# Optimization experiments

Measured on AMD Instinct MI355X. Metric: run time of the kernel, lower is better.

The kernel has to match this reference:

```python
import jax, jax.numpy as jnp
from jax import lax
import numpy as np

EPS = 1e-06


def conv1x1(x, W, b):
    # x: [B,C,H,W], W: [O,C], b: [O]
    return jnp.einsum('bchw,oc->bohw', x, W) + b[None, :, None, None]


def conv3x3(x, W, b):
    # W: [O,I,3,3], 'SAME' padding
    y = lax.conv_general_dilated(x, W, (1, 1), 'SAME',
                                 dimension_numbers=('NCHW', 'OIHW', 'NCHW'))
    return y + b[None, :, None, None]


def setup_inputs() -> dict:
    key = jax.random.key(0)
    ks = jax.random.split(key, 13)
    B, C, H, W = 8, 64, 256, 256
    kc, vc = 64, 64
    s = 0.05
    return {
        'x':  jax.random.normal(ks[0], (B, C, H, W), jnp.float32),
        'Wq': jax.random.normal(ks[1], (kc, C), jnp.float32) * s,
        'bq': jax.random.normal(ks[2], (kc,), jnp.float32) * s,
        'Wk': jax.random.normal(ks[3], (kc, C), jnp.float32) * s,
        'bk': jax.random.normal(ks[4], (kc,), jnp.float32) * s,
        'Wv': jax.random.normal(ks[5], (vc, C), jnp.float32) * s,
        'bv': jax.random.normal(ks[6], (vc,), jnp.float32) * s,
        'Wr': jax.random.normal(ks[7], (C, vc), jnp.float32) * s,
        'br': jax.random.normal(ks[8], (C,), jnp.float32) * s,
        'W1': jax.random.normal(ks[9], (C, C, 3, 3), jnp.float32) * s,
        'b1': jax.random.normal(ks[10], (C,), jnp.float32) * s,
        'W2': jax.random.normal(ks[11], (C, C, 3, 3), jnp.float32) * s,
        'b2': jax.random.normal(ks[12], (C,), jnp.float32) * s,
    }


def reference(x, Wq, bq, Wk, bk, Wv, bv, Wr, br, W1, b1, W2, b2):
    B, C, H, W = x.shape
    N = H * W
    kc = Wq.shape[0]
    vc = Wv.shape[0]

    Q = conv1x1(x, Wq, bq).reshape(B, kc, N)
    K = conv1x1(x, Wk, bk).reshape(B, kc, N)
    V = conv1x1(x, Wv, bv).reshape(B, vc, N)

    # L2-normalize over the channel axis (dim=-2 in torch)
    Qn = Q / jnp.linalg.norm(Q, axis=1, keepdims=True)   # [B,kc,N]
    Kn = K / jnp.linalg.norm(K, axis=1, keepdims=True)   # [B,kc,N]
    Qt = jnp.transpose(Qn, (0, 2, 1))                     # [B,N,kc]

    # denominator: 1 / (N + Q . (sum_n K + eps))
    k_sum = Kn.sum(axis=-1) + EPS                         # [B,kc]
    denom = 1.0 / (N + jnp.einsum('bnc,bc->bn', Qt, k_sum))  # [B,N]

    value_sum = V.sum(axis=-1, keepdims=True)             # [B,vc,1]

    # linear-attention aggregation: KV^T then Q.(KV)
    agg_kv = jnp.einsum('bmn,bcn->bmc', Kn, V)            # [B,kc,vc]
    # the per-batch/per-head torch loop sums head slices of the full kc
    # contraction -> equivalent to a single einsum over kc
    agg_qkv = jnp.einsum('bmc,bnm->bcn', agg_kv, Qt)      # [B,vc,N]

    numerator = value_sum + agg_qkv                       # [B,vc,N]
    weight_value = (numerator * denom[:, None, :]).reshape(B, vc, H, W)

    attn = conv1x1(weight_value, Wr, br)                  # [B,C,H,W]
    out = conv3x3(conv3x3(attn, W1, b1), W2, b2) * x + x
    return out
```

## Files before the change

kernel.cpp:

```cpp
#include <hip/hip_runtime.h>

typedef __attribute__((ext_vector_type(8))) short short8;
typedef __attribute__((ext_vector_type(4))) float f32x4;
typedef __attribute__((ext_vector_type(4))) int i32x4;

#define NPIX 65536
#define KPITCH 264
#define RED_KSUM 0
#define RED_VSUM 512
#define RED_AGG 1024

__device__ __forceinline__ float b2f(unsigned short u) {
  union { unsigned int i; float f; } z; z.i = ((unsigned int)u) << 16; return z.f;
}
__device__ __forceinline__ unsigned short f2b(float f) {
  union { float f; unsigned int i; } z; z.f = f;
  unsigned int r = z.i + 0x7fffu + ((z.i >> 16) & 1u);
  return (unsigned short)(r >> 16);
}
__device__ __forceinline__ unsigned int packbf(float a, float b) {
  return (unsigned int)f2b(a) | ((unsigned int)f2b(b) << 16);
}
__device__ __forceinline__ int cvtpk(float a, float b) {
  int r;
  asm("v_cvt_pk_bf16_f32 %0, %1, %2" : "=v"(r) : "v"(a), "v"(b));
  return r;
}

__global__ __launch_bounds__(256) void prep_kernel(
    const float* __restrict__ W1, const float* __restrict__ W2,
    const float* __restrict__ Wq, const float* __restrict__ Wk,
    const float* __restrict__ Wv,
    unsigned short* __restrict__ wA, unsigned short* __restrict__ wQKV,
    float* __restrict__ red)
{
  const int i = blockIdx.x * 256 + threadIdx.x;
  if (i < 73728) {
    const float* W = (i < 36864) ? W1 : W2;
    const int e = (i < 36864) ? i : (i - 36864);
    const int j    = e & 7;
    const int lane = (e >> 3) & 63;
    const int mt   = (e >> 9) & 3;
    const int kb   = (e >> 11) & 1;
    const int tap  = e >> 12;
    const int o = mt * 16 + (lane & 15);
    const int c = kb * 32 + ((lane >> 4) << 3) + j;
    wA[i] = f2b(W[o * 576 + c * 9 + tap]);
  } else if (i < 86016) {
    const int e = i - 73728;
    const int j    = e & 7;
    const int lane = (e >> 3) & 63;
    const int mt   = (e >> 9) & 3;
    const int kb   = (e >> 11) & 1;
    const int pj   = e >> 12;
    const float* W = (pj == 0) ? Wq : (pj == 1) ? Wk : Wv;
    const int o = mt * 16 + (lane & 15);
    const int c = kb * 32 + ((lane >> 4) << 3) + j;
    wQKV[e] = f2b(W[o * 64 + c]);
  } else if (i < 119808) {
    red[i - 86016] = 0.0f;
  }
}

#define PROJ(PIDX, BM)                                                         \
    {                                                                          \
      _Pragma("unroll")                                                        \
      for (int mt = 0; mt < 4; ++mt) {                                         \
        const f32x4 bb = *(const f32x4*)((BM) + mt * 16 + g * 4);              \
        _Pragma("unroll")                                                      \
        for (int nt = 0; nt < 4; ++nt) acc[mt][nt] = bb;                       \
      }                                                                        \
      _Pragma("unroll")                                                        \
      for (int kb = 0; kb < 2; ++kb) {                                         \
        const unsigned short* wp = wQKV + ((PIDX) * 2 + kb) * 2048 + l * 8;    \
        short8 af[4];                                                          \
        _Pragma("unroll")                                                      \
        for (int mt = 0; mt < 4; ++mt)                                         \
          af[mt] = *(const short8*)(wp + mt * 512);                            \
        _Pragma("unroll")                                                      \
        for (int mt = 0; mt < 4; ++mt)                                         \
          _Pragma("unroll")                                                    \
          for (int nt = 0; nt < 4; ++nt)                                       \
            acc[mt][nt] = __builtin_amdgcn_mfma_f32_16x16x32_bf16(             \
                af[mt], bf[nt][kb], acc[mt][nt], 0, 0, 0);                     \
      }                                                                        \
    }

__global__ __launch_bounds__(256, 2) void qkv_kernel(
    const float* __restrict__ x,
    const unsigned short* __restrict__ wQKV,
    const float* __restrict__ bq, const float* __restrict__ bk,
    const float* __restrict__ bv,
    unsigned short* __restrict__ Qn, float* __restrict__ red)
{
  __shared__ __align__(16) unsigned short sh[2 * 64 * KPITCH];
  unsigned short* ks = sh;
  unsigned short* vs = sh + 64 * KPITCH;
  unsigned int* shu = (unsigned int*)sh;
  const int b = blockIdx.y;
  const int t = threadIdx.x;
  const int w = t >> 6;
  const int l = t & 63;
  const int g = l >> 4;
  const int l15 = l & 15;
  const size_t xb = (size_t)b * 64 * NPIX;

  const f32x4 zero = {0.f, 0.f, 0.f, 0.f};
  f32x4 agg[4]  = {zero, zero, zero, zero};
  f32x4 kacc[4] = {zero, zero, zero, zero};
  f32x4 vacc[4] = {zero, zero, zero, zero};

  for (int it = 0; it < 4; ++it) {
    const int pxw = (blockIdx.x << 10) + (it << 8) + (w << 6);

    short8 bf[4][2];
#pragma unroll
    for (int nt = 0; nt < 4; ++nt) {
      const float* xp = x + xb + (size_t)(g * 8) * NPIX + pxw + nt * 16 + l15;
#pragma unroll
      for (int kb = 0; kb < 2; ++kb) {
        float f[8];
#pragma unroll
        for (int j = 0; j < 8; ++j)
          f[j] = xp[(size_t)(kb * 32 + j) * NPIX];
        union { i32x4 i; short8 s; } u;
        u.i.x = cvtpk(f[0], f[1]); u.i.y = cvtpk(f[2], f[3]);
        u.i.z = cvtpk(f[4], f[5]); u.i.w = cvtpk(f[6], f[7]);
        bf[nt][kb] = u.s;
      }
    }

    f32x4 acc[4][4];

    PROJ(0, bq);
    {
      float rq[4];
#pragma unroll
      for (int nt = 0; nt < 4; ++nt) {
        float ss = 0.f;
#pragma unroll
        for (int mt = 0; mt < 4; ++mt)
#pragma unroll
          for (int r = 0; r < 4; ++r)
            ss = fmaf(acc[mt][nt][r], acc[mt][nt][r], ss);
        ss += __shfl_xor(ss, 16);
        ss += __shfl_xor(ss, 32);
        rq[nt] = rsqrtf(ss);
      }
      unsigned int* sw = shu + w * 2304;
#pragma unroll
      for (int mt = 0; mt < 4; ++mt)
#pragma unroll
        for (int nt = 0; nt < 4; ++nt) {
          const int px = nt * 16 + l15;
          unsigned int* dst = sw + px * 36 + mt * 8 + g * 2;
          dst[0] = (unsigned)cvtpk(acc[mt][nt][0] * rq[nt], acc[mt][nt][1] * rq[nt]);
          dst[1] = (unsigned)cvtpk(acc[mt][nt][2] * rq[nt], acc[mt][nt][3] * rq[nt]);
        }
      const uint4* rr4 = (const uint4*)(shu + w * 2304);
#pragma unroll
      for (int k8 = 0; k8 < 8; ++k8) {
        const int p = (k8 << 3) + (l >> 3);
        const int ch8 = l & 7;
        *(uint4*)(Qn + ((size_t)b * NPIX + pxw + p) * 64 + ch8 * 8) =
            rr4[p * 9 + ch8];
      }
      __syncthreads();
    }

    PROJ(1, bk);
    {
      float rk[4];
#pragma unroll
      for (int nt = 0; nt < 4; ++nt) {
        float ss = 0.f;
#pragma unroll
        for (int mt = 0; mt < 4; ++mt)
#pragma unroll
          for (int r = 0; r < 4; ++r)
            ss = fmaf(acc[mt][nt][r], acc[mt][nt][r], ss);
        ss += __shfl_xor(ss, 16);
        ss += __shfl_xor(ss, 32);
        rk[nt] = rsqrtf(ss);
      }
#pragma unroll
      for (int mt = 0; mt < 4; ++mt)
#pragma unroll
        for (int nt = 0; nt < 4; ++nt)
#pragma unroll
          for (int r = 0; r < 4; ++r) {
            const float kn = acc[mt][nt][r] * rk[nt];
            kacc[mt][r] += kn;
            ks[(mt * 16 + g * 4 + r) * KPITCH + (w << 6) + nt * 16 + l15] =
                (unsigned short)cvtpk(kn, 0.f);
          }
    }

    PROJ(2, bv);
    {
#pragma unroll
      for (int mt = 0; mt < 4; ++mt)
#pragma unroll
        for (int nt = 0; nt < 4; ++nt)
#pragma unroll
          for (int r = 0; r < 4; ++r) {
            const float vv = acc[mt][nt][r];
            vacc[mt][r] += vv;
            vs[(mt * 16 + g * 4 + r) * KPITCH + (w << 6) + nt * 16 + l15] =
                (unsigned short)cvtpk(vv, 0.f);
          }
    }
    __syncthreads();

#pragma unroll
    for (int s = 0; s < 8; ++s) {
      const short8 ak =
          *(const short8*)(ks + (w * 16 + l15) * KPITCH + s * 32 + g * 8);
#pragma unroll
      for (int nt = 0; nt < 4; ++nt) {
        const short8 bv8 =
            *(const short8*)(vs + (nt * 16 + l15) * KPITCH + s * 32 + g * 8);
        agg[nt] = __builtin_amdgcn_mfma_f32_16x16x32_bf16(ak, bv8, agg[nt], 0, 0, 0);
      }
    }
    __syncthreads();
  }

#pragma unroll
  for (int mt = 0; mt < 4; ++mt)
#pragma unroll
    for (int r = 0; r < 4; ++r) {
      float kv = kacc[mt][r], vv = vacc[mt][r];
#pragma unroll
      for (int d = 1; d < 16; d <<= 1) {
        kv += __shfl_xor(kv, d);
        vv += __shfl_xor(vv, d);
      }
      if (l15 == 0) {
        atomicAdd(red + RED_KSUM + b * 64 + mt * 16 + g * 4 + r, kv);
        atomicAdd(red + RED_VSUM + b * 64 + mt * 16 + g * 4 + r, vv);
      }
    }
  float* ab = red + RED_AGG + b * 4096;
#pragma unroll
  for (int nt = 0; nt < 4; ++nt)
#pragma unroll
    for (int r = 0; r < 4; ++r)
      atomicAdd(ab + (w * 16 + g * 4 + r) * 64 + nt * 16 + l15, agg[nt][r]);
}

__global__ __launch_bounds__(256) void prep2_kernel(
    const float* __restrict__ Wr, const float* __restrict__ red,
    unsigned short* __restrict__ Cb, float* __restrict__ u,
    float* __restrict__ ks2)
{
  const int b = blockIdx.y;
  const int t = threadIdx.x;
  const int o = t & 63;
  const int kq = t >> 6;
  const float* wr = Wr + o * 64;
  const float* agg = red + RED_AGG + b * 4096;
#pragma unroll
  for (int i = 0; i < 4; ++i) {
    const int k = blockIdx.x * 16 + kq * 4 + i;
    const float* ar = agg + k * 64;
    float s = 0.f;
#pragma unroll
    for (int v = 0; v < 64; ++v) s = fmaf(wr[v], ar[v], s);
    const int mt = o >> 4, kb = k >> 5;
    const int lane = (o & 15) | (((k >> 3) & 3) << 4);
    const int j = k & 7;
    const unsigned short c1 = f2b(s);
    const float r1 = s - b2f(c1);
    Cb[b * 4096 + ((kb * 4 + mt) * 64 + lane) * 8 + j] = c1;
    Cb[32768 + b * 4096 + ((kb * 4 + mt) * 64 + lane) * 8 + j] = f2b(r1);
  }
  if (blockIdx.x == 0 && t < 64) {
    const float* vsr = red + RED_VSUM + b * 64;
    float s = 0.f;
#pragma unroll
    for (int v = 0; v < 64; ++v) s = fmaf(Wr[t * 64 + v], vsr[v], s);
    u[b * 64 + t] = s;
    ks2[b * 64 + t] = red[RED_KSUM + b * 64 + t] + 1e-6f;
  }
}

__global__ __launch_bounds__(256, 2) void attn_kernel(
    const unsigned short* __restrict__ Qn,
    const unsigned short* __restrict__ Cb,
    const float* __restrict__ u,
    const float* __restrict__ ks2,
    const float* __restrict__ br,
    unsigned short* __restrict__ attn)
{
  __shared__ __align__(16) unsigned short att[256 * 72];
  const int b = blockIdx.y;
  const int t = threadIdx.x;
  const int w = t >> 6, l = t & 63, g = l >> 4, l15 = l & 15;

  short8 af[2][2][4];
#pragma unroll
  for (int lvl = 0; lvl < 2; ++lvl)
#pragma unroll
    for (int kb = 0; kb < 2; ++kb)
#pragma unroll
      for (int mt = 0; mt < 4; ++mt)
        af[lvl][kb][mt] = *(const short8*)(
            Cb + lvl * 32768 + b * 4096 + ((kb * 4 + mt) * 64 + l) * 8);
  f32x4 uu[4], brf[4];
#pragma unroll
  for (int mt = 0; mt < 4; ++mt) {
    uu[mt]  = *(const f32x4*)(u + b * 64 + mt * 16 + g * 4);
    brf[mt] = *(const f32x4*)(br + mt * 16 + g * 4);
  }
  float ksl[16];
#pragma unroll
  for (int kb = 0; kb < 2; ++kb)
#pragma unroll
    for (int j = 0; j < 8; ++j)
      ksl[kb * 8 + j] = ks2[b * 64 + kb * 32 + g * 8 + j];

  for (int it = 0; it < 4; ++it) {
    const int pxw = (blockIdx.x << 10) + (it << 8) + (w << 6);
    short8 qf[4][2];
    float denom[4];
#pragma unroll
    for (int nt = 0; nt < 4; ++nt) {
      const unsigned short* qp =
          Qn + ((size_t)b * NPIX + pxw + nt * 16 + l15) * 64 + g * 8;
      qf[nt][0] = *(const short8*)qp;
      qf[nt][1] = *(const short8*)(qp + 32);
      float ss = 0.f;
#pragma unroll
      for (int kb = 0; kb < 2; ++kb)
#pragma unroll
        for (int j = 0; j < 8; ++j)
          ss = fmaf(b2f((unsigned short)qf[nt][kb][j]), ksl[kb * 8 + j], ss);
      ss += __shfl_xor(ss, 16);
      ss += __shfl_xor(ss, 32);
      denom[nt] = 1.0f / (65536.0f + ss);
    }
    f32x4 acc[4][4];
#pragma unroll
    for (int mt = 0; mt < 4; ++mt)
#pragma unroll
      for (int nt = 0; nt < 4; ++nt) acc[mt][nt] = uu[mt];
#pragma unroll
    for (int kb = 0; kb < 2; ++kb)
#pragma unroll
      for (int mt = 0; mt < 4; ++mt)
#pragma unroll
        for (int nt = 0; nt < 4; ++nt) {
          acc[mt][nt] = __builtin_amdgcn_mfma_f32_16x16x32_bf16(
              af[0][kb][mt], qf[nt][kb], acc[mt][nt], 0, 0, 0);
          acc[mt][nt] = __builtin_amdgcn_mfma_f32_16x16x32_bf16(
              af[1][kb][mt], qf[nt][kb], acc[mt][nt], 0, 0, 0);
        }
    unsigned int* sw = (unsigned int*)att + w * 2304;
#pragma unroll
    for (int mt = 0; mt < 4; ++mt)
#pragma unroll
      for (int nt = 0; nt < 4; ++nt) {
        const int px = nt * 16 + l15;
        unsigned int* dst = sw + px * 36 + mt * 8 + g * 2;
        dst[0] = (unsigned)cvtpk(fmaf(acc[mt][nt][0], denom[nt], brf[mt][0]),
                                 fmaf(acc[mt][nt][1], denom[nt], brf[mt][1]));
        dst[1] = (unsigned)cvtpk(fmaf(acc[mt][nt][2], denom[nt], brf[mt][2]),
                                 fmaf(acc[mt][nt][3], denom[nt], brf[mt][3]));
      }
    const uint4* rr4 = (const uint4*)att + w * 576;
#pragma unroll
    for (int k8 = 0; k8 < 8; ++k8) {
      const int p = (k8 << 3) + (l >> 3);
      const int ch8 = l & 7;
      *(uint4*)(attn + ((size_t)b * NPIX + pxw + p) * 64 + ch8 * 8) =
          rr4[p * 9 + ch8];
    }
  }
}

__global__ __launch_bounds__(512, 2) void fused_conv_kernel(
    const unsigned short* __restrict__ in,
    const unsigned short* __restrict__ wA,
    const float* __restrict__ b1, const float* __restrict__ b2,
    const float* __restrict__ xin,
    float* __restrict__ outf)
{
  __shared__ __align__(16) unsigned short mid[340 * 72];
  const int bz = blockIdx.z;
  const int ty0 = blockIdx.y << 3;
  const int tx0 = blockIdx.x << 5;
  const int tid = threadIdx.x;
  const int w = tid >> 6, lane = tid & 63, q = lane >> 4, l = lane & 15;
  const size_t nb = (size_t)bz * NPIX;

  if (w < 6) {
    f32x4 acc[4][4];
#pragma unroll
    for (int mt = 0; mt < 4; ++mt) {
      const f32x4 bb = *(const f32x4*)(b1 + mt * 16 + q * 4);
#pragma unroll
      for (int nt = 0; nt < 4; ++nt) acc[mt][nt] = bb;
    }
    int ylv[4], xlv[4];
#pragma unroll
    for (int nt = 0; nt < 4; ++nt) {
      const int mp = w * 64 + nt * 16 + l;
      const int mpc = mp < 340 ? mp : 339;
      ylv[nt] = mpc / 34;
      xlv[nt] = mpc - ylv[nt] * 34;
    }
    for (int tap = 0; tap < 9; ++tap) {
      const int dy = tap / 3, dx = tap - dy * 3;
#pragma unroll
      for (int kb = 0; kb < 2; ++kb) {
        const unsigned short* wp = wA + (tap * 2 + kb) * 2048 + lane * 8;
        short8 af[4];
#pragma unroll
        for (int mt = 0; mt < 4; ++mt) af[mt] = *(const short8*)(wp + mt * 512);
        short8 bfv[4];
#pragma unroll
        for (int nt = 0; nt < 4; ++nt) {
          const int gy = ty0 + ylv[nt] + dy - 2;
          const int gx = tx0 + xlv[nt] + dx - 2;
          short8 v = {0, 0, 0, 0, 0, 0, 0, 0};
          if ((unsigned)gy < 256u && (unsigned)gx < 256u)
            v = *(const short8*)(
                in + ((nb + (gy << 8) + gx) << 6) + ((kb * 4 + q) << 3));
          bfv[nt] = v;
        }
#pragma unroll
        for (int mt = 0; mt < 4; ++mt)
#pragma unroll
          for (int nt = 0; nt < 4; ++nt)
            acc[mt][nt] = __builtin_amdgcn_mfma_f32_16x16x32_bf16(
                af[mt], bfv[nt], acc[mt][nt], 0, 0, 0);
      }
    }
    unsigned int* mu = (unsigned int*)mid;
#pragma unroll
    for (int nt = 0; nt < 4; ++nt) {
      const int mp = w * 64 + nt * 16 + l;
      if (mp < 340) {
        const int gym = ty0 + ylv[nt] - 1;
        const int gxm = tx0 + xlv[nt] - 1;
        const bool ok = ((unsigned)gym < 256u) && ((unsigned)gxm < 256u);
#pragma unroll
        for (int mt = 0; mt < 4; ++mt) {
          unsigned int* dst = mu + mp * 36 + mt * 8 + q * 2;
          dst[0] = ok ? packbf(acc[mt][nt][0], acc[mt][nt][1]) : 0u;
          dst[1] = ok ? packbf(acc[mt][nt][2], acc[mt][nt][3]) : 0u;
        }
      }
    }
  }
  __syncthreads();

  f32x4 acc2[4][2];
#pragma unroll
  for (int mt = 0; mt < 4; ++mt) {
    const f32x4 bb = *(const f32x4*)(b2 + mt * 16 + q * 4);
    acc2[mt][0] = bb; acc2[mt][1] = bb;
  }
  const short8* tp2 = (const short8*)mid;
  const unsigned short* wA2p = wA + 36864;
  for (int tap = 0; tap < 9; ++tap) {
    const int dy = tap / 3, dx = tap - dy * 3;
#pragma unroll
    for (int kb = 0; kb < 2; ++kb) {
      const unsigned short* wp = wA2p + (tap * 2 + kb) * 2048 + lane * 8;
      short8 af[4];
#pragma unroll
      for (int mt = 0; mt < 4; ++mt) af[mt] = *(const short8*)(wp + mt * 512);
      short8 bf2[2];
#pragma unroll
      for (int nt = 0; nt < 2; ++nt) {
        const int yl = w + dy;
        const int xl = nt * 16 + l + dx;
        bf2[nt] = tp2[(yl * 34 + xl) * 9 + (kb << 2) + q];
      }
#pragma unroll
      for (int mt = 0; mt < 4; ++mt)
#pragma unroll
        for (int nt = 0; nt < 2; ++nt)
          acc2[mt][nt] = __builtin_amdgcn_mfma_f32_16x16x32_bf16(
              af[mt], bf2[nt], acc2[mt][nt], 0, 0, 0);
    }
  }
#pragma unroll
  for (int mt = 0; mt < 4; ++mt)
#pragma unroll
    for (int nt = 0; nt < 2; ++nt) {
      const int gx = tx0 + nt * 16 + l;
      const int gy = ty0 + w;
#pragma unroll
      for (int r = 0; r < 4; ++r) {
        const int o = (mt << 4) + (q << 2) + r;
        const size_t idx = (((size_t)bz * 64 + o) << 16) + (gy << 8) + gx;
        const float xo = xin[idx];
        outf[idx] = fmaf(acc2[mt][nt][r], xo, xo);
      }
    }
}

extern "C" void kernel_launch(void* const* d_in, const int* in_sizes, int n_in,
                              void* d_out, int out_size, void* d_ws, size_t ws_size,
                              hipStream_t stream) {
  (void)in_sizes; (void)n_in; (void)out_size; (void)ws_size;
  const float* x  = (const float*)d_in[0];
  const float* Wq = (const float*)d_in[1];
  const float* bq = (const float*)d_in[2];
  const float* Wk = (const float*)d_in[3];
  const float* bk = (const float*)d_in[4];
  const float* Wv = (const float*)d_in[5];
  const float* bv = (const float*)d_in[6];
  const float* Wr = (const float*)d_in[7];
  const float* br = (const float*)d_in[8];
  const float* W1 = (const float*)d_in[9];
  const float* b1 = (const float*)d_in[10];
  const float* W2 = (const float*)d_in[11];
  const float* b2 = (const float*)d_in[12];

  unsigned short* wA1  = (unsigned short*)d_ws;
  unsigned short* wQKV = (unsigned short*)((char*)d_ws + 147456);
  unsigned short* Cb   = (unsigned short*)((char*)d_ws + 147456);
  float* u_  = (float*)((char*)d_ws + 278528);
  float* ks2 = (float*)((char*)d_ws + 280576);
  float* red = (float*)((char*)d_ws + 282624);
  unsigned short* bufB = (unsigned short*)((char*)d_ws + 282624);
  unsigned short* bufQ = (unsigned short*)((char*)d_out + 67108864);

  prep_kernel<<<468, 256, 0, stream>>>(W1, W2, Wq, Wk, Wv, wA1, wQKV, red);
  qkv_kernel<<<dim3(64, 8), 256, 0, stream>>>(x, wQKV, bq, bk, bv, bufQ, red);
  prep2_kernel<<<dim3(4, 8), 256, 0, stream>>>(Wr, red, Cb, u_, ks2);
  attn_kernel<<<dim3(64, 8), 256, 0, stream>>>(bufQ, Cb, u_, ks2, br, bufB);
  fused_conv_kernel<<<dim3(8, 32, 8), 512, 0, stream>>>(
      bufB, wA1, b1, b2, x, (float*)d_out);
}
```

Measured before the change: 561.2 us.

## Fuse attention output into the conv kernel with halo recompute in LDS

Merges the attention kernel into the fused 3x3 conv kernel. Each block now computes the attention output for its 36x12 haloed tile straight into LDS, and conv1 reads from LDS instead of global memory. This removes the bf16 attention buffer write and read plus one launch, at the cost of recomputing the halo pixels and reloading the Cb weights from global per tile. prep2 now uses one block per batch with the aggregation staged in shared memory, and the workspace layout is reshuffled. The larger LDS footprint and the launch_bounds(512,4) request may limit occupancy or cause register spills.

After: 642.7 us. 1.15x slower.

```diff
diff --git a/kernel.cpp b/kernel.cpp
--- a/kernel.cpp
+++ b/kernel.cpp
@@ -254,16 +254,21 @@
     unsigned short* __restrict__ Cb, float* __restrict__ u,
     float* __restrict__ ks2)
 {
-  const int b = blockIdx.y;
+  __shared__ float sagg[4096];
+  __shared__ float skv[128];
+  const int b = blockIdx.x;
   const int t = threadIdx.x;
+  const float* aggg = red + RED_AGG + b * 4096;
+  for (int i = t; i < 4096; i += 256) sagg[i] = aggg[i];
+  if (t < 64) skv[t] = red[RED_KSUM + b * 64 + t];
+  else if (t < 128) skv[t] = red[RED_VSUM + b * 64 + (t - 64)];
+  __syncthreads();
   const int o = t & 63;
   const int kq = t >> 6;
   const float* wr = Wr + o * 64;
-  const float* agg = red + RED_AGG + b * 4096;
-#pragma unroll
-  for (int i = 0; i < 4; ++i) {
-    const int k = blockIdx.x * 16 + kq * 4 + i;
-    const float* ar = agg + k * 64;
+  for (int i = 0; i < 16; ++i) {
+    const int k = kq * 16 + i;
+    const float* ar = sagg + k * 64;
     float s = 0.f;
 #pragma unroll
     for (int v = 0; v < 64; ++v) s = fmaf(wr[v], ar[v], s);
@@ -275,134 +280,117 @@
     Cb[b * 4096 + ((kb * 4 + mt) * 64 + lane) * 8 + j] = c1;
     Cb[32768 + b * 4096 + ((kb * 4 + mt) * 64 + lane) * 8 + j] = f2b(r1);
   }
-  if (blockIdx.x == 0 && t < 64) {
-    const float* vsr = red + RED_VSUM + b * 64;
+  if (t < 64) {
     float s = 0.f;
 #pragma unroll
-    for (int v = 0; v < 64; ++v) s = fmaf(Wr[t * 64 + v], vsr[v], s);
+    for (int v = 0; v < 64; ++v) s = fmaf(Wr[t * 64 + v], skv[64 + v], s);
     u[b * 64 + t] = s;
-    ks2[b * 64 + t] = red[RED_KSUM + b * 64 + t] + 1e-6f;
-  }
-}
-
-__global__ __launch_bounds__(256, 2) void attn_kernel(
+    ks2[b * 64 + t] = skv[t] + 1e-6f;
+  }
+}
+
+__global__ __launch_bounds__(512, 4) void mega_kernel(
     const unsigned short* __restrict__ Qn,
     const unsigned short* __restrict__ Cb,
     const float* __restrict__ u,
     const float* __restrict__ ks2,
     const float* __restrict__ br,
-    unsigned short* __restrict__ attn)
-{
-  __shared__ __align__(16) unsigned short att[256 * 72];
-  const int b = blockIdx.y;
-  const int t = threadIdx.x;
-  const int w = t >> 6, l = t & 63, g = l >> 4, l15 = l & 15;
-
-  short8 af[2][2][4];
-#pragma unroll
-  for (int lvl = 0; lvl < 2; ++lvl)
-#pragma unroll
-    for (int kb = 0; kb < 2; ++kb)
-#pragma unroll
-      for (int mt = 0; mt < 4; ++mt)
-        af[lvl][kb][mt] = *(const short8*)(
-            Cb + lvl * 32768 + b * 4096 + ((kb * 4 + mt) * 64 + l) * 8);
-  f32x4 uu[4], brf[4];
-#pragma unroll
-  for (int mt = 0; mt < 4; ++mt) {
-    uu[mt]  = *(const f32x4*)(u + b * 64 + mt * 16 + g * 4);
-    brf[mt] = *(const f32x4*)(br + mt * 16 + g * 4);
-  }
-  float ksl[16];
-#pragma unroll
-  for (int kb = 0; kb < 2; ++kb)
-#pragma unroll
-    for (int j = 0; j < 8; ++j)
-      ksl[kb * 8 + j] = ks2[b * 64 + kb * 32 + g * 8 + j];
-
-  for (int it = 0; it < 4; ++it) {
-    const int pxw = (blockIdx.x << 10) + (it << 8) + (w << 6);
-    short8 qf[4][2];
-    float denom[4];
-#pragma unroll
-    for (int nt = 0; nt < 4; ++nt) {
-      const unsigned short* qp =
-          Qn + ((size_t)b * NPIX + pxw + nt * 16 + l15) * 64 + g * 8;
-      qf[nt][0] = *(const short8*)qp;
-      qf[nt][1] = *(const short8*)(qp + 32);
-      float ss = 0.f;
-#pragma unroll
-      for (int kb = 0; kb < 2; ++kb)
-#pragma unroll
-        for (int j = 0; j < 8; ++j)
-          ss = fmaf(b2f((unsigned short)qf[nt][kb][j]), ksl[kb * 8 + j], ss);
-      ss += __shfl_xor(ss, 16);
-      ss += __shfl_xor(ss, 32);
-      denom[nt] = 1.0f / (65536.0f + ss);
-    }
-    f32x4 acc[4][4];
-#pragma unroll
-    for (int mt = 0; mt < 4; ++mt)
-#pragma unroll
-      for (int nt = 0; nt < 4; ++nt) acc[mt][nt] = uu[mt];
-#pragma unroll
-    for (int kb = 0; kb < 2; ++kb)
-#pragma unroll
-      for (int mt = 0; mt < 4; ++mt)
-#pragma unroll
-        for (int nt = 0; nt < 4; ++nt) {
-          acc[mt][nt] = __builtin_amdgcn_mfma_f32_16x16x32_bf16(
-              af[0][kb][mt], qf[nt][kb], acc[mt][nt], 0, 0, 0);
-          acc[mt][nt] = __builtin_amdgcn_mfma_f32_16x16x32_bf16(
-              af[1][kb][mt], qf[nt][kb], acc[mt][nt], 0, 0, 0);
-        }
-    unsigned int* sw = (unsigned int*)att + w * 2304;
-#pragma unroll
-    for (int mt = 0; mt < 4; ++mt)
-#pragma unroll
-      for (int nt = 0; nt < 4; ++nt) {
-        const int px = nt * 16 + l15;
-        unsigned int* dst = sw + px * 36 + mt * 8 + g * 2;
-        dst[0] = (unsigned)cvtpk(fmaf(acc[mt][nt][0], denom[nt], brf[mt][0]),
-                                 fmaf(acc[mt][nt][1], denom[nt], brf[mt][1]));
-        dst[1] = (unsigned)cvtpk(fmaf(acc[mt][nt][2], denom[nt], brf[mt][2]),
-                                 fmaf(acc[mt][nt][3], denom[nt], brf[mt][3]));
-      }
-    const uint4* rr4 = (const uint4*)att + w * 576;
-#pragma unroll
-    for (int k8 = 0; k8 < 8; ++k8) {
-      const int p = (k8 << 3) + (l >> 3);
-      const int ch8 = l & 7;
-      *(uint4*)(attn + ((size_t)b * NPIX + pxw + p) * 64 + ch8 * 8) =
-          rr4[p * 9 + ch8];
-    }
-  }
-}
-
-__global__ __launch_bounds__(512, 2) void fused_conv_kernel(
-    const unsigned short* __restrict__ in,
     const unsigned short* __restrict__ wA,
     const float* __restrict__ b1, const float* __restrict__ b2,
     const float* __restrict__ xin,
     float* __restrict__ outf)
 {
-  __shared__ __align__(16) unsigned short mid[340 * 72];
+  __shared__ __align__(16) unsigned short lds[432 * 72];
   const int bz = blockIdx.z;
   const int ty0 = blockIdx.y << 3;
   const int tx0 = blockIdx.x << 5;
   const int tid = threadIdx.x;
   const int w = tid >> 6, lane = tid & 63, q = lane >> 4, l = lane & 15;
   const size_t nb = (size_t)bz * NPIX;
-
+  unsigned int* mu = (unsigned int*)lds;
+
+  if (w < 7) {
+    float ksl[16];
+#pragma unroll
+    for (int kb = 0; kb < 2; ++kb)
+#pragma unroll
+      for (int j = 0; j < 8; ++j)
+        ksl[kb * 8 + j] = ks2[bz * 64 + kb * 32 + q * 8 + j];
+    f32x4 brf[4];
+#pragma unroll
+    for (int mt = 0; mt < 4; ++mt)
+      brf[mt] = *(const f32x4*)(br + mt * 16 + q * 4);
+
+#pragma unroll
+    for (int nt = 0; nt < 4; ++nt) {
+      const int mp = w * 64 + nt * 16 + l;
+      const int iy = mp / 36;
+      const int ix = mp - iy * 36;
+      const int gy = ty0 + iy - 2;
+      const int gx = tx0 + ix - 2;
+      const bool okimg = ((unsigned)gy < 256u) && ((unsigned)gx < 256u);
+      short8 qf0 = {0, 0, 0, 0, 0, 0, 0, 0};
+      short8 qf1 = {0, 0, 0, 0, 0, 0, 0, 0};
+      if (okimg && mp < 432) {
+        const unsigned short* qp = Qn + ((nb + (gy << 8) + gx) << 6) + (q << 3);
+        qf0 = *(const short8*)qp;
+        qf1 = *(const short8*)(qp + 32);
+      }
+      float ss = 0.f;
+#pragma unroll
+      for (int j = 0; j < 8; ++j)
+        ss = fmaf(b2f((unsigned short)qf0[j]), ksl[j], ss);
+#pragma unroll
+      for (int j = 0; j < 8; ++j)
+        ss = fmaf(b2f((unsigned short)qf1[j]), ksl[8 + j], ss);
+      ss += __shfl_xor(ss, 16);
+      ss += __shfl_xor(ss, 32);
+      const float denom = 1.0f / (65536.0f + ss);
+      f32x4 acc[4];
+#pragma unroll
+      for (int mt = 0; mt < 4; ++mt)
+        acc[mt] = *(const f32x4*)(u + bz * 64 + mt * 16 + q * 4);
+#pragma unroll
+      for (int lvl = 0; lvl < 2; ++lvl)
+#pragma unroll
+        for (int kb = 0; kb < 2; ++kb) {
+          const unsigned short* cp =
+              Cb + lvl * 32768 + bz * 4096 + ((kb * 4) * 64 + lane) * 8;
+          const short8 qv = kb ? qf1 : qf0;
+#pragma unroll
+          for (int mt = 0; mt < 4; ++mt) {
+            const short8 af = *(const short8*)(cp + mt * 512);
+            acc[mt] = __builtin_amdgcn_mfma_f32_16x16x32_bf16(
+                af, qv, acc[mt], 0, 0, 0);
+          }
+        }
+      if (mp < 432) {
+        unsigned int* dst = mu + mp * 36 + q * 2;
+#pragma unroll
+        for (int mt = 0; mt < 4; ++mt) {
+          const unsigned a0 = okimg
+              ? (unsigned)cvtpk(fmaf(acc[mt][0], denom, brf[mt][0]),
+                                fmaf(acc[mt][1], denom, brf[mt][1])) : 0u;
+          const unsigned a1 = okimg
+              ? (unsigned)cvtpk(fmaf(acc[mt][2], denom, brf[mt][2]),
+                                fmaf(acc[mt][3], denom, brf[mt][3])) : 0u;
+          dst[mt * 8] = a0;
+          dst[mt * 8 + 1] = a1;
+        }
+      }
+    }
+  }
+  __syncthreads();
+
+  f32x4 acc1[4][4];
+  int ylv[4], xlv[4];
   if (w < 6) {
-    f32x4 acc[4][4];
 #pragma unroll
     for (int mt = 0; mt < 4; ++mt) {
       const f32x4 bb = *(const f32x4*)(b1 + mt * 16 + q * 4);
 #pragma unroll
-      for (int nt = 0; nt < 4; ++nt) acc[mt][nt] = bb;
-    }
-    int ylv[4], xlv[4];
+      for (int nt = 0; nt < 4; ++nt) acc1[mt][nt] = bb;
+    }
 #pragma unroll
     for (int nt = 0; nt < 4; ++nt) {
       const int mp = w * 64 + nt * 16 + l;
@@ -410,6 +398,7 @@
       ylv[nt] = mpc / 34;
       xlv[nt] = mpc - ylv[nt] * 34;
     }
+    const short8* tpIn = (const short8*)lds;
     for (int tap = 0; tap < 9; ++tap) {
       const int dy = tap / 3, dx = tap - dy * 3;
 #pragma unroll
@@ -420,24 +409,21 @@
         for (int mt = 0; mt < 4; ++mt) af[mt] = *(const short8*)(wp + mt * 512);
         short8 bfv[4];
 #pragma unroll
-        for (int nt = 0; nt < 4; ++nt) {
-          const int gy = ty0 + ylv[nt] + dy - 2;
-          const int gx = tx0 + xlv[nt] + dx - 2;
-          short8 v = {0, 0, 0, 0, 0, 0, 0, 0};
-          if ((unsigned)gy < 256u && (unsigned)gx < 256u)
-            v = *(const short8*)(
-                in + ((nb + (gy << 8) + gx) << 6) + ((kb * 4 + q) << 3));
-          bfv[nt] = v;
-        }
+        for (int nt = 0; nt < 4; ++nt)
+          bfv[nt] = tpIn[((ylv[nt] + dy) * 36 + (xlv[nt] + dx)) * 9 +
+                         (kb << 2) + q];
 #pragma unroll
         for (int mt = 0; mt < 4; ++mt)
 #pragma unroll
           for (int nt = 0; nt < 4; ++nt)
-            acc[mt][nt] = __builtin_amdgcn_mfma_f32_16x16x32_bf16(
-                af[mt], bfv[nt], acc[mt][nt], 0, 0, 0);
-      }
-    }
-    unsigned int* mu = (unsigned int*)mid;
+            acc1[mt][nt] = __builtin_amdgcn_mfma_f32_16x16x32_bf16(
+                af[mt], bfv[nt], acc1[mt][nt], 0, 0, 0);
+      }
+    }
+  }
+  __syncthreads();
+
+  if (w < 6) {
 #pragma unroll
     for (int nt = 0; nt < 4; ++nt) {
       const int mp = w * 64 + nt * 16 + l;
@@ -448,8 +434,8 @@
 #pragma unroll
         for (int mt = 0; mt < 4; ++mt) {
           unsigned int* dst = mu + mp * 36 + mt * 8 + q * 2;
-          dst[0] = ok ? packbf(acc[mt][nt][0], acc[mt][nt][1]) : 0u;
-          dst[1] = ok ? packbf(acc[mt][nt][2], acc[mt][nt][3]) : 0u;
+          dst[0] = ok ? packbf(acc1[mt][nt][0], acc1[mt][nt][1]) : 0u;
+          dst[1] = ok ? packbf(acc1[mt][nt][2], acc1[mt][nt][3]) : 0u;
         }
       }
     }
@@ -462,7 +448,7 @@
     const f32x4 bb = *(const f32x4*)(b2 + mt * 16 + q * 4);
     acc2[mt][0] = bb; acc2[mt][1] = bb;
   }
-  const short8* tp2 = (const short8*)mid;
+  const short8* tp2 = (const short8*)lds;
   const unsigned short* wA2p = wA + 36864;
   for (int tap = 0; tap < 9; ++tap) {
     const int dy = tap / 3, dx = tap - dy * 3;
@@ -521,19 +507,17 @@
   const float* W2 = (const float*)d_in[11];
   const float* b2 = (const float*)d_in[12];
 
-  unsigned short* wA1  = (unsigned short*)d_ws;
-  unsigned short* wQKV = (unsigned short*)((char*)d_ws + 147456);
-  unsigned short* Cb   = (unsigned short*)((char*)d_ws + 147456);
-  float* u_  = (float*)((char*)d_ws + 278528);
-  float* ks2 = (float*)((char*)d_ws + 280576);
-  float* red = (float*)((char*)d_ws + 282624);
-  unsigned short* bufB = (unsigned short*)((char*)d_ws + 282624);
-  unsigned short* bufQ = (unsigned short*)((char*)d_out + 67108864);
+  unsigned short* wA1 = (unsigned short*)d_ws;
+  float* red = (float*)((char*)d_ws + 147456);
+  float* u_  = (float*)((char*)d_ws + 147456);
+  float* ks2 = (float*)((char*)d_ws + 147456 + 2048);
+  unsigned short* Cb = (unsigned short*)((char*)d_ws + 147456 + 4096);
+  unsigned short* Qn = (unsigned short*)((char*)d_ws + 282624);
+  unsigned short* wQKV = (unsigned short*)((char*)d_out + 67108864);
 
   prep_kernel<<<468, 256, 0, stream>>>(W1, W2, Wq, Wk, Wv, wA1, wQKV, red);
-  qkv_kernel<<<dim3(64, 8), 256, 0, stream>>>(x, wQKV, bq, bk, bv, bufQ, red);
-  prep2_kernel<<<dim3(4, 8), 256, 0, stream>>>(Wr, red, Cb, u_, ks2);
-  attn_kernel<<<dim3(64, 8), 256, 0, stream>>>(bufQ, Cb, u_, ks2, br, bufB);
-  fused_conv_kernel<<<dim3(8, 32, 8), 512, 0, stream>>>(
-      bufB, wA1, b1, b2, x, (float*)d_out);
-}
+  qkv_kernel<<<dim3(64, 8), 256, 0, stream>>>(x, wQKV, bq, bk, bv, Qn, red);
+  prep2_kernel<<<8, 256, 0, stream>>>(Wr, red, Cb, u_, ks2);
+  mega_kernel<<<dim3(8, 32, 8), 512, 0, stream>>>(
+      Qn, Cb, u_, ks2, br, wA1, b1, b2, x, (float*)d_out);
+}
```
